# Optimization experiments

Measured on AMD Instinct MI355X. Metric: run time of the kernel, lower is better.

The kernel has to match this reference:

```python
import jax, jax.numpy as jnp
import numpy as np

GAMMA = 2.0
NUM_CLASSES = 33

def _cdist(x):
    # pairwise euclidean distance per batch: x [B,N,C] -> [B,N,N]
    sq = jnp.sum(x * x, axis=-1)                      # [B,N]
    d2 = sq[:, :, None] + sq[:, None, :] - 2.0 * jnp.einsum('bnc,bmc->bnm', x, x)
    d2 = jnp.maximum(d2, 0.0)
    d = jnp.sqrt(jnp.where(d2 > 0, d2, 1.0))          # safe sqrt (zero-distance -> 0, no nan grad)
    return jnp.where(d2 > 0, d, 0.0)


def setup_inputs() -> dict:
    key = jax.random.key(0)
    k1, k2, k3 = jax.random.split(key, 3)
    B, N, C = 2, 4096, NUM_CLASSES
    predictions = jax.random.normal(k1, (B, N, C), dtype=jnp.float32)
    targets = jax.random.randint(k2, (B, N), 0, C, dtype=jnp.int32)
    y_ohe = jax.nn.one_hot(targets, C, dtype=jnp.float32)
    pred_choice = jax.random.randint(k3, (B, N), 0, C, dtype=jnp.int32)
    return {"predictions": predictions, "y_ohe": y_ohe, "targets": targets, "pred_choice": pred_choice}


def reference(predictions, y_ohe, targets, pred_choice):
    B, N, C = predictions.shape
    # cross-entropy (mean over all B*N positions, no class weights)
    logp = jax.nn.log_softmax(predictions, axis=-1)                       # [B,N,C]
    logp_t = jnp.take_along_axis(logp, targets[..., None].astype(jnp.int32), axis=-1)[..., 0]
    ce_loss = -jnp.mean(logp_t)                                           # scalar

    # distance-map KL term
    dis_map = _cdist(y_ohe)                                               # [B,N,N]
    dis_map = jnp.where(dis_map > 1.0, 0.9, dis_map)
    dis_map = jnp.where(dis_map < 1.0, 0.05, dis_map)
    pred_prob = jax.nn.softmax(predictions, axis=-1)
    pred_map = _cdist(pred_prob)                                          # [B,N,N]
    # torch F.kl_div(input, target) with default 'mean': mean(target*(log(target)-input))
    dis_map_loss = jnp.mean(dis_map * (jnp.log(dis_map) - pred_map))

    # focal weighting of the (scalar) CE loss
    pn = jnp.take_along_axis(jnp.exp(logp), targets[..., None].astype(jnp.int32), axis=-1)[..., 0]
    pn = pn.reshape(-1)                                                   # [B*N]
    loss = jnp.mean((1.0 - pn) ** GAMMA * ce_loss)

    # dice loss: per-class loop collapses exactly to a global match count
    eps = 1.0
    matches = jnp.sum((targets.reshape(-1) == pred_choice.reshape(-1)).astype(jnp.float32))
    total = targets.size
    dice = 1.0 - 2.0 * ((matches + eps) / (2.0 * total + eps))

    return loss + dice + dis_map_loss
```

## Files before the change

### kernel.cpp

```cpp
#include <hip/hip_runtime.h>
#include <math.h>

#define BB 2
#define NN 4096
#define CC 33
#define RP 40
#define TILE 64
#define NTILES (NN / TILE)
#define NPB 1056
#define ROWBLK 256
#define PAIRBLK (BB * NPB)
#define NSLOT 64
#define SLOTSTR 32

typedef __attribute__((ext_vector_type(8))) short frag_ab;
typedef __attribute__((ext_vector_type(4))) float f32x4;

__device__ __forceinline__ float fast_sqrt(float x) {
    return __builtin_amdgcn_sqrtf(x);
}
__device__ __forceinline__ unsigned f2bf(float x) {
    unsigned u = __float_as_uint(x);
    return (u + 0x7FFFu + ((u >> 16) & 1u)) >> 16;
}
__device__ __forceinline__ float bf2f(unsigned b) {
    return __uint_as_float(b << 16);
}

__global__ __launch_bounds__(256) void row_kernel(
    const float* __restrict__ pred, const int* __restrict__ targets,
    const int* __restrict__ pred_choice, unsigned short* __restrict__ p16,
    float* __restrict__ sqn, float2* __restrict__ part_row,
    int* __restrict__ part_match, float* __restrict__ slotf,
    unsigned* __restrict__ subcnt, unsigned* __restrict__ master)
{
    __shared__ __align__(16) float sraw[32 * CC];
    __shared__ float2 lds_cf[4];
    __shared__ int lds_mt[4];

    if (blockIdx.x == 0) {
        for (int i = threadIdx.x; i < NSLOT * SLOTSTR; i += 256) {
            slotf[i] = 0.0f;
            subcnt[i] = 0u;
        }
        if (threadIdx.x == 0) *master = 0u;
    }

    {
        const float4* src = (const float4*)(pred + (size_t)blockIdx.x * 32 * CC);
        float4* dst = (float4*)sraw;
        for (int k = threadIdx.x; k < 264; k += 256) dst[k] = src[k];
    }
    __syncthreads();

    int l = threadIdx.x & 63;
    int w = threadIdx.x >> 6;
    int r = l >> 3;
    int c = l & 7;
    int rloc = w * 8 + r;
    int row = blockIdx.x * 32 + rloc;

    float v[4];
    #pragma unroll
    for (int k = 0; k < 4; k++) v[k] = sraw[rloc * CC + 4 * c + k];
    float v32 = sraw[rloc * CC + 32];

    float m = fmaxf(fmaxf(v[0], v[1]), fmaxf(v[2], v[3]));
    if (c == 0) m = fmaxf(m, v32);
    m = fmaxf(m, __shfl_xor(m, 1));
    m = fmaxf(m, __shfl_xor(m, 2));
    m = fmaxf(m, __shfl_xor(m, 4));

    float e[4];
    float s = 0.0f;
    #pragma unroll
    for (int k = 0; k < 4; k++) { e[k] = __expf(v[k] - m); s += e[k]; }
    float e32 = __expf(v32 - m);
    if (c == 0) s += e32;
    s += __shfl_xor(s, 1);
    s += __shfl_xor(s, 2);
    s += __shfl_xor(s, 4);
    float inv = 1.0f / s;

    unsigned pb[4];
    float sq = 0.0f;
    #pragma unroll
    for (int k = 0; k < 4; k++) {
        pb[k] = f2bf(e[k] * inv);
        float pf = bf2f(pb[k]);
        sq += pf * pf;
    }
    unsigned c32u = f2bf(e32 * inv);
    float c32 = bf2f(c32u);
    if (c == 0) sq += c32 * c32;
    sq += __shfl_xor(sq, 1);
    sq += __shfl_xor(sq, 2);
    sq += __shfl_xor(sq, 4);

    {
        uint2 st = make_uint2(pb[0] | (pb[1] << 16), pb[2] | (pb[3] << 16));
        *(uint2*)&p16[(size_t)row * RP + 4 * c] = st;
    }
    if (c == 0) {
        uint4 st = make_uint4(c32u, 0u, 0u, 0u);
        *(uint4*)&p16[(size_t)row * RP + 32] = st;
        sqn[row] = sq;
    }

    int tg = targets[row];
    float cand = 0.0f;
    if (tg < 32) {
        int cc = tg >> 2, kk = tg & 3;
        if (cc == c) cand = e[kk];
    } else if (c == 0) cand = e32;
    cand += __shfl_xor(cand, 1);
    cand += __shfl_xor(cand, 2);
    cand += __shfl_xor(cand, 4);

    float ce = 0.0f, fo = 0.0f; int mt = 0;
    if (c == 0) {
        float pt = cand * inv;
        ce = -__logf(pt);
        float om = 1.0f - pt;
        fo = om * om;
        mt = (tg == pred_choice[row]) ? 1 : 0;
    }
    ce += __shfl_xor(ce, 8);  ce += __shfl_xor(ce, 16);  ce += __shfl_xor(ce, 32);
    fo += __shfl_xor(fo, 8);  fo += __shfl_xor(fo, 16);  fo += __shfl_xor(fo, 32);
    mt += __shfl_xor(mt, 8);  mt += __shfl_xor(mt, 16);  mt += __shfl_xor(mt, 32);

    if (l == 0) { lds_cf[w] = make_float2(ce, fo); lds_mt[w] = mt; }
    __syncthreads();
    if (threadIdx.x == 0) {
        float2 a = lds_cf[0], b2 = lds_cf[1], c2 = lds_cf[2], d = lds_cf[3];
        part_row[blockIdx.x] = make_float2(a.x + b2.x + c2.x + d.x,
                                           a.y + b2.y + c2.y + d.y);
        part_match[blockIdx.x] = lds_mt[0] + lds_mt[1] + lds_mt[2] + lds_mt[3];
    }
}

__global__ __launch_bounds__(256) void pair_kernel(
    const unsigned short* __restrict__ p16, const float* __restrict__ sqn,
    const float2* __restrict__ part_row, const int* __restrict__ part_match,
    float* __restrict__ slotf, unsigned* __restrict__ subcnt,
    unsigned* __restrict__ master, float* __restrict__ out)
{
    __shared__ __align__(16) unsigned short spi[TILE * RP];
    __shared__ __align__(16) unsigned short spj[2][TILE * RP];
    __shared__ float ssqi[TILE], ssqj[2][TILE];
    __shared__ float red[4];
    __shared__ int lastFlag;
    __shared__ double lds_ce[4], lds_fo[4], lds_pr[4];
    __shared__ int lds_mt[4];

    int bid = blockIdx.x;
    int b = bid / NPB;
    int t = bid % NPB;

    int p = (int)(32.5f - fast_sqrt(fmaxf(1056.25f - (float)t, 0.0f)));
    if (p < 0) p = 0;
    if (p > 31) p = 31;
    while (p > 0 && p * (65 - p) > t) --p;
    while (p < 31 && (p + 1) * (64 - p) <= t) ++p;
    int rem = t - p * (65 - p);
    int c0 = 32 - p;
    int ti = 2 * p + (rem >= c0);
    int u = (rem >= c0) ? rem - c0 : rem;
    int tjA = ti + 2 * u;
    bool hasB = (tjA + 1 < NTILES);
    bool diagA = (tjA == ti);

    int i0 = ti * TILE, j0A = tjA * TILE;

    const float4* srci  = (const float4*)(p16 + ((size_t)b * NN + i0) * RP);
    const float4* srcjA = (const float4*)(p16 + ((size_t)b * NN + j0A) * RP);
    float4* di  = (float4*)spi;
    float4* djA = (float4*)spj[0];
    for (int k = threadIdx.x; k < TILE * (RP / 8); k += 256) {
        di[k]  = srci[k];
        djA[k] = srcjA[k];
    }
    if (hasB) {
        const float4* srcjB = srcjA + TILE * (RP / 8);
        float4* djB = (float4*)spj[1];
        for (int k = threadIdx.x; k < TILE * (RP / 8); k += 256)
            djB[k] = srcjB[k];
    }
    if (threadIdx.x < TILE)
        ssqi[threadIdx.x] = sqn[b * NN + i0 + threadIdx.x];
    else if (threadIdx.x < 2 * TILE)
        ssqj[0][threadIdx.x - TILE] = sqn[b * NN + j0A + (threadIdx.x - TILE)];
    else if (hasB && threadIdx.x < 3 * TILE)
        ssqj[1][threadIdx.x - 2 * TILE] = sqn[b * NN + j0A + TILE + (threadIdx.x - 2 * TILE)];
    __syncthreads();

    int l = threadIdx.x & 63;
    int w = threadIdx.x >> 6;
    int col = l & 15;
    int kc = l >> 4;

    frag_ab afr = *(const frag_ab*)&spi[(16 * w + col) * RP + kc * 8];

    float qi[4], c32a[4];
    #pragma unroll
    for (int r = 0; r < 4; r++) {
        int ir = 16 * w + kc * 4 + r;
        qi[r]   = ssqi[ir];
        c32a[r] = bf2f(spi[ir * RP + 32]);
    }
    int gi0 = i0 + 16 * w + kc * 4;

    float ssum = 0.0f;

    #pragma unroll
    for (int jt = 0; jt < 2; jt++) {
        if (jt == 1 && !hasB) break;
        const unsigned short* spjx = spj[jt];
        const float* ssqx = ssqj[jt];
        int j0 = j0A + jt * TILE;
        bool dg = (jt == 0) && diagA;

        #pragma unroll
        for (int n = 0; n < 4; n++) {
            frag_ab bfr = *(const frag_ab*)&spjx[(16 * n + col) * RP + kc * 8];
            f32x4 acc = {0.0f, 0.0f, 0.0f, 0.0f};
            acc = __builtin_amdgcn_mfma_f32_16x16x32_bf16(afr, bfr, acc, 0, 0, 0);

            float c32b = bf2f(spjx[(16 * n + col) * RP + 32]);
            float qj   = ssqx[16 * n + col];
            int   gj   = j0 + 16 * n + col;

            #pragma unroll
            for (int r = 0; r < 4; r++) {
                float g  = fmaf(c32a[r], c32b, acc[r]);
                float d2 = fmaf(-2.0f, g, qi[r] + qj);
                float d  = fast_sqrt(fmaxf(d2, 0.0f));
                ssum += (!dg || gj > gi0 + r) ? d : 0.0f;
            }
        }
    }

    #pragma unroll
    for (int off = 32; off; off >>= 1) ssum += __shfl_xor(ssum, off);
    if (l == 0) red[w] = ssum;
    __syncthreads();

    if (threadIdx.x == 0) {
        float blockSum = red[0] + red[1] + red[2] + red[3];
        int slot = (bid & (NSLOT - 1)) * SLOTSTR;
        __hip_atomic_fetch_add(&slotf[slot], blockSum,
                               __ATOMIC_RELAXED, __HIP_MEMORY_SCOPE_AGENT);
        asm volatile("s_waitcnt vmcnt(0)" ::: "memory");
        unsigned o = __hip_atomic_fetch_add(&subcnt[slot], 1u,
                                            __ATOMIC_RELAXED, __HIP_MEMORY_SCOPE_AGENT);
        int last = 0;
        if (o == (PAIRBLK / NSLOT) - 1) {
            unsigned o2 = __hip_atomic_fetch_add(master, 1u,
                                                 __ATOMIC_RELAXED, __HIP_MEMORY_SCOPE_AGENT);
            last = (o2 == NSLOT - 1);
        }
        lastFlag = last;
    }
    __syncthreads();
    if (!lastFlag) return;

    double ce = 0.0, fo = 0.0, pr = 0.0;
    int mt = 0;
    for (int i = threadIdx.x; i < ROWBLK; i += 256) {
        float2 v = part_row[i];
        ce += (double)v.x;
        fo += (double)v.y;
        mt += part_match[i];
    }
    for (int i = threadIdx.x; i < NSLOT; i += 256)
        pr += (double)__hip_atomic_load(&slotf[i * SLOTSTR],
                                        __ATOMIC_RELAXED, __HIP_MEMORY_SCOPE_AGENT);

    #pragma unroll
    for (int off = 32; off; off >>= 1) {
        ce += __shfl_xor(ce, off);
        fo += __shfl_xor(fo, off);
        pr += __shfl_xor(pr, off);
        mt += __shfl_xor(mt, off);
    }
    if (l == 0) { lds_ce[w] = ce; lds_fo[w] = fo; lds_pr[w] = pr; lds_mt[w] = mt; }
    __syncthreads();
    if (threadIdx.x == 0) {
        double tce = lds_ce[0] + lds_ce[1] + lds_ce[2] + lds_ce[3];
        double tfo = lds_fo[0] + lds_fo[1] + lds_fo[2] + lds_fo[3];
        double tpr = lds_pr[0] + lds_pr[1] + lds_pr[2] + lds_pr[3];
        int    tmt = lds_mt[0] + lds_mt[1] + lds_mt[2] + lds_mt[3];

        double BN = (double)(BB * NN);
        double loss = (tce / BN) * (tfo / BN);
        double dice = 1.0 - 2.0 * ((double)tmt + 1.0) / (2.0 * BN + 1.0);
        double S = 2.0 * tpr;
        double mean_pred = S / (BN * (double)NN);
        double dml = 0.05 * log(0.05) - 0.05 * mean_pred;
        out[0] = (float)(loss + dice + dml);
    }
}

extern "C" void kernel_launch(void* const* d_in, const int* in_sizes, int n_in,
                              void* d_out, int out_size, void* d_ws, size_t ws_size,
                              hipStream_t stream)
{
    const float* pred        = (const float*)d_in[0];
    const int*   targets     = (const int*)d_in[2];
    const int*   pred_choice = (const int*)d_in[3];

    char* ws = (char*)d_ws;
    size_t off = 0;
    unsigned short* p16 = (unsigned short*)ws;
    off += (size_t)BB * NN * RP * sizeof(unsigned short);
    float* sqn = (float*)(ws + off);
    off += (size_t)BB * NN * sizeof(float);
    off = (off + 127) & ~(size_t)127;
    float2* part_row = (float2*)(ws + off);
    off += (size_t)ROWBLK * sizeof(float2);
    int* part_match = (int*)(ws + off);
    off += (size_t)ROWBLK * sizeof(int);
    off = (off + 127) & ~(size_t)127;
    float* slotf = (float*)(ws + off);
    off += (size_t)NSLOT * SLOTSTR * sizeof(float);
    unsigned* subcnt = (unsigned*)(ws + off);
    off += (size_t)NSLOT * SLOTSTR * sizeof(unsigned);
    unsigned* master = (unsigned*)(ws + off);
    off += sizeof(unsigned);

    row_kernel<<<ROWBLK, 256, 0, stream>>>(pred, targets, pred_choice,
                                           p16, sqn, part_row, part_match,
                                           slotf, subcnt, master);
    pair_kernel<<<PAIRBLK, 256, 0, stream>>>(p16, sqn, part_row, part_match,
                                             slotf, subcnt, master, (float*)d_out);
}
```

Baseline: 21.21 us.

## Process three j-tiles per pair block and pack squared norms into padded rows

Each pair block now covers up to three j-tiles against one i-tile instead of two, which cuts the block count from 1056 to 715 per batch and reuses the i-tile fragments across more work. The squared norm is stored in the padding of each bf16 row, so the separate sqn array and its loads are gone. The tile mapping now uses a simple serial loop instead of the closed-form sqrt index, and the completion counter per slot is adjusted for uneven block distribution. Fewer blocks may reduce occupancy balance and lengthen the tail on the GPU.

```diff
diff --git a/kernel.cpp b/kernel.cpp
--- a/kernel.cpp
+++ b/kernel.cpp
@@ -7,7 +7,7 @@
 #define RP 40
 #define TILE 64
 #define NTILES (NN / TILE)
-#define NPB 1056
+#define NPB 715
 #define ROWBLK 256
 #define PAIRBLK (BB * NPB)
 #define NSLOT 64
@@ -30,9 +30,9 @@
 __global__ __launch_bounds__(256) void row_kernel(
     const float* __restrict__ pred, const int* __restrict__ targets,
     const int* __restrict__ pred_choice, unsigned short* __restrict__ p16,
-    float* __restrict__ sqn, float2* __restrict__ part_row,
-    int* __restrict__ part_match, float* __restrict__ slotf,
-    unsigned* __restrict__ subcnt, unsigned* __restrict__ master)
+    float2* __restrict__ part_row, int* __restrict__ part_match,
+    float* __restrict__ slotf, unsigned* __restrict__ subcnt,
+    unsigned* __restrict__ master)
 {
     __shared__ __align__(16) float sraw[32 * CC];
     __shared__ float2 lds_cf[4];
@@ -102,9 +102,8 @@
         *(uint2*)&p16[(size_t)row * RP + 4 * c] = st;
     }
     if (c == 0) {
-        uint4 st = make_uint4(c32u, 0u, 0u, 0u);
+        uint4 st = make_uint4(c32u, __float_as_uint(sq), 0u, 0u);
         *(uint4*)&p16[(size_t)row * RP + 32] = st;
-        sqn[row] = sq;
     }
 
     int tg = targets[row];
@@ -140,14 +139,13 @@
 }
 
 __global__ __launch_bounds__(256) void pair_kernel(
-    const unsigned short* __restrict__ p16, const float* __restrict__ sqn,
+    const unsigned short* __restrict__ p16,
     const float2* __restrict__ part_row, const int* __restrict__ part_match,
     float* __restrict__ slotf, unsigned* __restrict__ subcnt,
     unsigned* __restrict__ master, float* __restrict__ out)
 {
     __shared__ __align__(16) unsigned short spi[TILE * RP];
-    __shared__ __align__(16) unsigned short spj[2][TILE * RP];
-    __shared__ float ssqi[TILE], ssqj[2][TILE];
+    __shared__ __align__(16) unsigned short spj[3 * TILE * RP];
     __shared__ float red[4];
     __shared__ int lastFlag;
     __shared__ double lds_ce[4], lds_fo[4], lds_pr[4];
@@ -157,41 +155,22 @@
     int b = bid / NPB;
     int t = bid % NPB;
 
-    int p = (int)(32.5f - fast_sqrt(fmaxf(1056.25f - (float)t, 0.0f)));
-    if (p < 0) p = 0;
-    if (p > 31) p = 31;
-    while (p > 0 && p * (65 - p) > t) --p;
-    while (p < 31 && (p + 1) * (64 - p) <= t) ++p;
-    int rem = t - p * (65 - p);
-    int c0 = 32 - p;
-    int ti = 2 * p + (rem >= c0);
-    int u = (rem >= c0) ? rem - c0 : rem;
-    int tjA = ti + 2 * u;
-    bool hasB = (tjA + 1 < NTILES);
+    int ti = 0, rem = t;
+    while (rem >= (NTILES - ti + 2) / 3) { rem -= (NTILES - ti + 2) / 3; ++ti; }
+    int tjA = ti + 3 * rem;
+    int avail = NTILES - tjA; if (avail > 3) avail = 3;
     bool diagA = (tjA == ti);
-
     int i0 = ti * TILE, j0A = tjA * TILE;
 
-    const float4* srci  = (const float4*)(p16 + ((size_t)b * NN + i0) * RP);
-    const float4* srcjA = (const float4*)(p16 + ((size_t)b * NN + j0A) * RP);
-    float4* di  = (float4*)spi;
-    float4* djA = (float4*)spj[0];
-    for (int k = threadIdx.x; k < TILE * (RP / 8); k += 256) {
-        di[k]  = srci[k];
-        djA[k] = srcjA[k];
-    }
-    if (hasB) {
-        const float4* srcjB = srcjA + TILE * (RP / 8);
-        float4* djB = (float4*)spj[1];
-        for (int k = threadIdx.x; k < TILE * (RP / 8); k += 256)
-            djB[k] = srcjB[k];
-    }
-    if (threadIdx.x < TILE)
-        ssqi[threadIdx.x] = sqn[b * NN + i0 + threadIdx.x];
-    else if (threadIdx.x < 2 * TILE)
-        ssqj[0][threadIdx.x - TILE] = sqn[b * NN + j0A + (threadIdx.x - TILE)];
-    else if (hasB && threadIdx.x < 3 * TILE)
-        ssqj[1][threadIdx.x - 2 * TILE] = sqn[b * NN + j0A + TILE + (threadIdx.x - 2 * TILE)];
+    {
+        const float4* srci = (const float4*)(p16 + ((size_t)b * NN + i0) * RP);
+        const float4* srcj = (const float4*)(p16 + ((size_t)b * NN + j0A) * RP);
+        float4* di = (float4*)spi;
+        float4* dj = (float4*)spj;
+        int jf4 = avail * 320;
+        for (int k = threadIdx.x; k < 320; k += 256) di[k] = srci[k];
+        for (int k = threadIdx.x; k < jf4; k += 256) dj[k] = srcj[k];
+    }
     __syncthreads();
 
     int l = threadIdx.x & 63;
@@ -205,7 +184,7 @@
     #pragma unroll
     for (int r = 0; r < 4; r++) {
         int ir = 16 * w + kc * 4 + r;
-        qi[r]   = ssqi[ir];
+        qi[r]   = __uint_as_float(*(const unsigned*)&spi[ir * RP + 34]);
         c32a[r] = bf2f(spi[ir * RP + 32]);
     }
     int gi0 = i0 + 16 * w + kc * 4;
@@ -213,22 +192,22 @@
     float ssum = 0.0f;
 
     #pragma unroll
-    for (int jt = 0; jt < 2; jt++) {
-        if (jt == 1 && !hasB) break;
-        const unsigned short* spjx = spj[jt];
-        const float* ssqx = ssqj[jt];
+    for (int jt = 0; jt < 3; jt++) {
+        if (jt >= avail) break;
+        const unsigned short* spjx = spj + jt * TILE * RP;
         int j0 = j0A + jt * TILE;
         bool dg = (jt == 0) && diagA;
 
         #pragma unroll
         for (int n = 0; n < 4; n++) {
-            frag_ab bfr = *(const frag_ab*)&spjx[(16 * n + col) * RP + kc * 8];
+            int jr = 16 * n + col;
+            frag_ab bfr = *(const frag_ab*)&spjx[jr * RP + kc * 8];
             f32x4 acc = {0.0f, 0.0f, 0.0f, 0.0f};
             acc = __builtin_amdgcn_mfma_f32_16x16x32_bf16(afr, bfr, acc, 0, 0, 0);
 
-            float c32b = bf2f(spjx[(16 * n + col) * RP + 32]);
-            float qj   = ssqx[16 * n + col];
-            int   gj   = j0 + 16 * n + col;
+            float c32b = bf2f(spjx[jr * RP + 32]);
+            float qj   = __uint_as_float(*(const unsigned*)&spjx[jr * RP + 34]);
+            int   gj   = j0 + jr - col + col;
 
             #pragma unroll
             for (int r = 0; r < 4; r++) {
@@ -247,14 +226,16 @@
 
     if (threadIdx.x == 0) {
         float blockSum = red[0] + red[1] + red[2] + red[3];
-        int slot = (bid & (NSLOT - 1)) * SLOTSTR;
+        int slotIdx = bid & (NSLOT - 1);
+        int slot = slotIdx * SLOTSTR;
+        unsigned expect = (unsigned)(PAIRBLK / NSLOT) + (slotIdx < (PAIRBLK % NSLOT) ? 1u : 0u);
         __hip_atomic_fetch_add(&slotf[slot], blockSum,
                                __ATOMIC_RELAXED, __HIP_MEMORY_SCOPE_AGENT);
         asm volatile("s_waitcnt vmcnt(0)" ::: "memory");
         unsigned o = __hip_atomic_fetch_add(&subcnt[slot], 1u,
                                             __ATOMIC_RELAXED, __HIP_MEMORY_SCOPE_AGENT);
         int last = 0;
-        if (o == (PAIRBLK / NSLOT) - 1) {
+        if (o == expect - 1) {
             unsigned o2 = __hip_atomic_fetch_add(master, 1u,
                                                  __ATOMIC_RELAXED, __HIP_MEMORY_SCOPE_AGENT);
             last = (o2 == NSLOT - 1);
@@ -313,8 +294,6 @@
     size_t off = 0;
     unsigned short* p16 = (unsigned short*)ws;
     off += (size_t)BB * NN * RP * sizeof(unsigned short);
-    float* sqn = (float*)(ws + off);
-    off += (size_t)BB * NN * sizeof(float);
     off = (off + 127) & ~(size_t)127;
     float2* part_row = (float2*)(ws + off);
     off += (size_t)ROWBLK * sizeof(float2);
@@ -329,8 +308,8 @@
     off += sizeof(unsigned);
 
     row_kernel<<<ROWBLK, 256, 0, stream>>>(pred, targets, pred_choice,
-                                           p16, sqn, part_row, part_match,
+                                           p16, part_row, part_match,
                                            slotf, subcnt, master);
-    pair_kernel<<<PAIRBLK, 256, 0, stream>>>(p16, sqn, part_row, part_match,
+    pair_kernel<<<PAIRBLK, 256, 0, stream>>>(p16, part_row, part_match,
                                              slotf, subcnt, master, (float*)d_out);
 }
```

After: 20.13 us. 5.1% less time.
